# Kernel tuning notes

Hardware: AMD Instinct MI355X
Metric: run time of the kernel (lower is better)

The kernel has to match this reference:

```python
import jax, jax.numpy as jnp
import numpy as np

# pywt db4 reconstruction low-pass (rec_lo) coefficients.
_H = np.array([
    0.23037781330885523, 0.7148465705525415, 0.6308807679295904,
    -0.02798376941698385, -0.18703481171888114, 0.030841381835986965,
    0.032883011666982945, -0.010597401784997278], dtype=np.float64)
# pywt dec_lo = _H[::-1]; conv (flipped) correlation kernel = dec_lo[::-1] = _H.
_FLO = _H
# dec_hi[k] = (-1)^(7-k) * _H[k]; correlation kernel = dec_hi[::-1] -> (-1)^k * _H[7-k].
_FHI = np.array([(-1.0) ** k * _H[7 - k] for k in range(8)])
_FILT = jnp.asarray(np.stack([_FLO, _FHI])[:, None, :], dtype=jnp.float32)  # [2,1,8]
_PAD = 7  # filter_len - 1
_LEVEL = 4


def _dwt_step(sig):
    """One pywt dwt level, mode='symmetric'. sig: [N, L] -> (cA, cD), each [N, (L+7)//2]."""
    # symmetric (half-sample) extension by filter_len-1 each side, drop first sample
    # so that stride-2 VALID correlation reproduces pywt's output phase/length.
    xp = jnp.pad(sig, ((0, 0), (_PAD, _PAD)), mode='symmetric')[:, 1:]
    out = jax.lax.conv_general_dilated(
        xp[:, None, :], _FILT, window_strides=(2,), padding='VALID',
        dimension_numbers=('NCH', 'OIH', 'NCH'))  # [N, 2, (L+7)//2]
    return out[:, 0, :], out[:, 1, :]


def setup_inputs() -> dict:
    key = jax.random.key(0)
    x = jax.random.normal(key, (64, 4096, 32), dtype=jnp.float32)  # [B, L, C]
    return {"x": x}


def reference(x):
    """Faithful batched version of pywt.wavedec(x[i,:,j], 'db4', 'symmetric', level=4).
    Returns tuple (cA4, cD4, cD3, cD2, cD1), each [B, C, scale_len]."""
    B, L, C = x.shape
    sig = jnp.transpose(x, (0, 2, 1)).reshape(B * C, L)
    details = []
    for _ in range(_LEVEL):
        sig, cd = _dwt_step(sig)
        details.append(cd)
    coeffs = [sig] + details[::-1]  # [cA_L, cD_L, ..., cD_1] like pywt.wavedec
    return tuple(c.reshape(B, C, c.shape[-1]) for c in coeffs)
```

## Files before the change

kernel.cpp:

```cpp
#include <hip/hip_runtime.h>


#define NT 256
#define NCHB 2

#define LPX 634
#define LP1 322
#define LP2 166
#define LP3 86
#define CDP1 314
#define CDP2 154
#define CDP3 82
#define CDP4 40
#define CAP4 40

#define L0C 4096
#define L1C 2051
#define L2C 1029
#define L3C 518
#define L4C 262
#define SC 2048

#define OFF_CD4 ((size_t)SC * L4C)
#define OFF_CD3 ((size_t)2 * SC * L4C)
#define OFF_CD2 (OFF_CD3 + (size_t)SC * L3C)
#define OFF_CD1 (OFF_CD2 + (size_t)SC * L2C)

__device__ __forceinline__ void filt8(
    const float w0, const float w1, const float w2, const float w3,
    const float w4, const float w5, const float w6, const float w7,
    float& a, float& d) {
    constexpr float FLO[8] = {
        0.23037781330885523f,  0.7148465705525415f,  0.6308807679295904f,
        -0.02798376941698385f, -0.18703481171888114f, 0.030841381835986965f,
        0.032883011666982945f, -0.010597401784997278f};
    constexpr float FHI[8] = {
        -0.010597401784997278f, -0.032883011666982945f, 0.030841381835986965f,
        0.18703481171888114f,  -0.02798376941698385f,  -0.6308807679295904f,
        0.7148465705525415f,   -0.23037781330885523f};
    float a0 = FLO[0] * w0;
    a0 = fmaf(FLO[1], w1, a0); a0 = fmaf(FLO[2], w2, a0); a0 = fmaf(FLO[3], w3, a0);
    float a1 = FLO[4] * w4;
    a1 = fmaf(FLO[5], w5, a1); a1 = fmaf(FLO[6], w6, a1); a1 = fmaf(FLO[7], w7, a1);
    a = a0 + a1;
    float d0 = FHI[0] * w0;
    d0 = fmaf(FHI[1], w1, d0); d0 = fmaf(FHI[2], w2, d0); d0 = fmaf(FHI[3], w3, d0);
    float d1 = FHI[4] * w4;
    d1 = fmaf(FHI[5], w5, d1); d1 = fmaf(FHI[6], w6, d1); d1 = fmaf(FHI[7], w7, d1);
    d = d0 + d1;
}

template <int R, bool LAST>
__device__ __forceinline__ void level_run(
    const float* __restrict__ src, int PS, int srclo,
    float* __restrict__ dst, int PD, int DL,
    int lo, int hi,
    float* __restrict__ cdbuf, int CDP,
    float* __restrict__ cabuf,
    int c, int slot) {
    const int span = hi - lo;
    int i0r = slot * R;
    if (i0r > span - R) i0r = span - R;
    const int i0 = lo + i0r;

    const float2* row2 = reinterpret_cast<const float2*>(src + c * PS);
    int p = i0 - (srclo >> 1);
    float2 f0 = row2[p], f1 = row2[p + 1], f2 = row2[p + 2];
    float* drow = LAST ? nullptr : dst + c * PD;
    float* cdrow = cdbuf + c * CDP - lo;
    float* carow = LAST ? cabuf + c * CAP4 - lo : nullptr;

#pragma unroll
    for (int r = 0; r < R; ++r) {
        const float2 f3 = row2[p + 3 + r];
        const int i = i0 + r;
        float a, d;
        filt8(f0.x, f0.y, f1.x, f1.y, f2.x, f2.y, f3.x, f3.y, a, d);

        if constexpr (!LAST) {
            drow[i - lo + 6] = a;
            if (lo == 0 && i < 6) drow[5 - i] = a;
            if (hi == DL && i >= DL - 7) drow[(2 * DL - 1 - i) - lo + 6] = a;
        } else {
            carow[i] = a;
        }
        cdrow[i] = d;
        f0 = f1; f1 = f2; f2 = f3;
    }
}

__device__ __forceinline__ void dump_rows(
    const float* __restrict__ buf, int pitch, int bufLo,
    float* __restrict__ gbase, int rowLen, int ownLo, int ownHi, int tid) {
    const int span = ownHi - ownLo;
#pragma unroll
    for (int c2 = 0; c2 < NCHB; ++c2) {
        float* g = gbase + (size_t)c2 * rowLen + ownLo;
        const float* s = buf + c2 * pitch + (ownLo - bufLo);
        for (int i = tid; i < span; i += NT) g[i] = s[i];
    }
}

__global__ __launch_bounds__(NT, 8) void fused_dwt_kernel(
    const float* __restrict__ x, float* __restrict__ out) {
    __shared__ __align__(16) float bx[NCHB * LPX];
    __shared__ __align__(16) float b1[NCHB * LP1];
    __shared__ __align__(16) float b2[NCHB * LP2];
    __shared__ __align__(16) float b3[NCHB * LP3];
    __shared__ __align__(16) float cd1[NCHB * CDP1];
    __shared__ __align__(16) float cd2[NCHB * CDP2];
    __shared__ __align__(16) float cd3[NCHB * CDP3];
    __shared__ __align__(16) float cd4[NCHB * CDP4];
    __shared__ __align__(16) float ca4[NCHB * CAP4];

    const int bid = blockIdx.x;
    const int work = (bid & 7) * 1024 + (bid >> 3);
    const int cg = work & 15;
    const int tile = (work >> 4) & 7;
    const int b = work >> 7;

    const int tid = threadIdx.x;
    const int c = tid & 1;
    const int slot = tid >> 1;
    const int c0 = cg * 2;
    const int sigB = b * 32 + c0;

    const int lo4 = 33 * tile, hi4 = min(L4C, lo4 + 33);
    const int lo3 = max(0, 2 * lo4 - 6), hi3 = min(L3C, 2 * hi4);
    const int lo2 = max(0, 2 * lo3 - 6), hi2 = min(L2C, 2 * hi3);
    const int lo1 = max(0, 2 * lo2 - 6), hi1 = min(L1C, 2 * hi2);
    const int lox = max(0, 2 * lo1 - 6), hix = min(L0C, 2 * hi1);

    const float* xb = x + (size_t)b * (L0C * 32) + c0;
    const int npair = (hix - lox) >> 1;
    for (int q = tid; q < npair; q += NT) {
        const int j = q << 1;
        const int t = lox + j;
        const float2 va = *reinterpret_cast<const float2*>(xb + (size_t)t * 32);
        const float2 vb = *reinterpret_cast<const float2*>(xb + (size_t)(t + 1) * 32);
        const float avv[2] = {va.x, va.y};
        const float bvv[2] = {vb.x, vb.y};
#pragma unroll
        for (int hh = 0; hh < NCHB; ++hh)
            *reinterpret_cast<float2*>(bx + hh * LPX + 6 + j) = make_float2(avv[hh], bvv[hh]);
        if (lox == 0 && t < 6) {
#pragma unroll
            for (int hh = 0; hh < NCHB; ++hh) {
                bx[hh * LPX + 5 - t] = avv[hh];
                if (t + 1 < 6) bx[hh * LPX + 4 - t] = bvv[hh];
            }
        }
        if (hix == L0C && t + 1 >= L0C - 7) {
#pragma unroll
            for (int hh = 0; hh < NCHB; ++hh) {
                if (t >= L0C - 7) bx[hh * LPX + (2 * L0C - 1 - t) - lox + 6] = avv[hh];
                bx[hh * LPX + (2 * L0C - 2 - t) - lox + 6] = bvv[hh];
            }
        }
    }
    __syncthreads();

    float* gca4 = out + (size_t)sigB * L4C;
    float* gcd4 = out + OFF_CD4 + (size_t)sigB * L4C;
    float* gcd3 = out + OFF_CD3 + (size_t)sigB * L3C;
    float* gcd2 = out + OFF_CD2 + (size_t)sigB * L2C;
    float* gcd1 = out + OFF_CD1 + (size_t)sigB * L1C;

    const int o1lo = tile ? 264 * tile - 34 : 0;
    const int o1hi = (tile == 7) ? L1C : 264 * tile + 230;
    const int o2lo = tile ? 132 * tile - 10 : 0;
    const int o2hi = (tile == 7) ? L2C : 132 * tile + 122;
    const int o3lo = tile ? 66 * tile - 2 : 0;
    const int o3hi = (tile == 7) ? L3C : 66 * tile + 64;

    level_run<3, false>(bx, LPX, lox, b1, LP1, L1C, lo1, hi1, cd1, CDP1, nullptr, c, slot);
    __syncthreads();
    level_run<2, false>(b1, LP1, lo1, b2, LP2, L2C, lo2, hi2, cd2, CDP2, nullptr, c, slot);
    __syncthreads();
    level_run<1, false>(b2, LP2, lo2, b3, LP3, L3C, lo3, hi3, cd3, CDP3, nullptr, c, slot);
    __syncthreads();
    level_run<1, true>(b3, LP3, lo3, nullptr, 0, L4C, lo4, hi4, cd4, CDP4, ca4, c, slot);
    __syncthreads();

    dump_rows(cd1, CDP1, lo1, gcd1, L1C, o1lo, o1hi, tid);
    dump_rows(cd2, CDP2, lo2, gcd2, L2C, o2lo, o2hi, tid);
    dump_rows(cd3, CDP3, lo3, gcd3, L3C, o3lo, o3hi, tid);
    dump_rows(cd4, CDP4, lo4, gcd4, L4C, lo4, hi4, tid);
    dump_rows(ca4, CAP4, lo4, gca4, L4C, lo4, hi4, tid);
}

extern "C" void kernel_launch(void* const* d_in, const int* in_sizes, int n_in,
                              void* d_out, int out_size, void* d_ws, size_t ws_size,
                              hipStream_t stream) {
    (void)in_sizes; (void)n_in; (void)d_ws; (void)ws_size; (void)out_size;
    const float* x = (const float*)d_in[0];
    float* out = (float*)d_out;
    fused_dwt_kernel<<<dim3(8192), dim3(NT), 0, stream>>>(x, out);
}
```

Baseline: 32.90 us.

## Process four channels per block with larger per-thread runs and interleaved stores

Each block now handles four channels instead of two, halving the grid and loading input as float4 rows. Per-thread run lengths grow to 6/4/2/2 outputs with paired float2 LDS writes and a tail path. Boundary mirroring is specialised to edge tiles only via a template flag. Each level's detail coefficients are written to global memory right after its barrier, so the writes overlap later levels; occupancy hint drops to 5 waves because LDS use doubles.

New measurement: 30.11 us. -8.5%, faster.

```diff
diff --git a/kernel.cpp b/kernel.cpp
--- a/kernel.cpp
+++ b/kernel.cpp
@@ -2,7 +2,7 @@
 
 
 #define NT 256
-#define NCHB 2
+#define NCHB 4
 
 #define LPX 634
 #define LP1 322
@@ -21,10 +21,10 @@
 #define L4C 262
 #define SC 2048
 
-#define OFF_CD4 ((size_t)SC * L4C)
-#define OFF_CD3 ((size_t)2 * SC * L4C)
-#define OFF_CD2 (OFF_CD3 + (size_t)SC * L3C)
-#define OFF_CD1 (OFF_CD2 + (size_t)SC * L2C)
+#define OFF_CD4 (SC * L4C)
+#define OFF_CD3 (2 * SC * L4C)
+#define OFF_CD2 (OFF_CD3 + SC * L3C)
+#define OFF_CD1 (OFF_CD2 + SC * L2C)
 
 __device__ __forceinline__ void filt8(
     const float w0, const float w1, const float w2, const float w3,
@@ -50,7 +50,7 @@
     d = d0 + d1;
 }
 
-template <int R, bool LAST>
+template <int R, bool MG, bool LAST>
 __device__ __forceinline__ void level_run(
     const float* __restrict__ src, int PS, int srclo,
     float* __restrict__ dst, int PD, int DL,
@@ -58,34 +58,67 @@
     float* __restrict__ cdbuf, int CDP,
     float* __restrict__ cabuf,
     int c, int slot) {
+    static_assert((R & 1) == 0, "R must be even");
     const int span = hi - lo;
-    int i0r = slot * R;
-    if (i0r > span - R) i0r = span - R;
-    const int i0 = lo + i0r;
-
-    const float2* row2 = reinterpret_cast<const float2*>(src + c * PS);
-    int p = i0 - (srclo >> 1);
+    const int nrun = span / R;
+    bool tail = false;
+    int i0;
+    if (slot < nrun) {
+        i0 = lo + slot * R;
+    } else if (slot == nrun && nrun * R < span) {
+        i0 = lo + ((span - R) & ~1);
+        tail = (span & 1) != 0;
+    } else {
+        return;
+    }
+
+    const float* rowb = src + c * PS;
+    const float2* row2 = reinterpret_cast<const float2*>(rowb);
+    const int p = i0 - (srclo >> 1);
     float2 f0 = row2[p], f1 = row2[p + 1], f2 = row2[p + 2];
-    float* drow = LAST ? nullptr : dst + c * PD;
-    float* cdrow = cdbuf + c * CDP - lo;
-    float* carow = LAST ? cabuf + c * CAP4 - lo : nullptr;
-
+
+    float* dbase = LAST ? nullptr : dst + c * PD;
+    float* cdbase = cdbuf + c * CDP;
+    float* cabase = LAST ? cabuf + c * CAP4 : nullptr;
+
+    float ap = 0.f, dp = 0.f;
 #pragma unroll
     for (int r = 0; r < R; ++r) {
         const float2 f3 = row2[p + 3 + r];
         const int i = i0 + r;
         float a, d;
         filt8(f0.x, f0.y, f1.x, f1.y, f2.x, f2.y, f3.x, f3.y, a, d);
-
+        if (r & 1) {
+            const int w = i - 1 - lo;
+            if constexpr (!LAST)
+                *reinterpret_cast<float2*>(dbase + w + 6) = make_float2(ap, a);
+            else
+                *reinterpret_cast<float2*>(cabase + w) = make_float2(ap, a);
+            *reinterpret_cast<float2*>(cdbase + w) = make_float2(dp, d);
+        } else {
+            ap = a; dp = d;
+        }
+        if constexpr (MG && !LAST) {
+            if (lo == 0 && i < 6) dbase[5 - i] = a;
+            if (hi == DL && i >= DL - 7) dbase[(2 * DL - 1 - i) - lo + 6] = a;
+        }
+        f0 = f1; f1 = f2; f2 = f3;
+    }
+    if (tail) {
+        const int i = hi - 1;
+        const float* s = rowb + 6 - srclo;
+        float a, d;
+        filt8(s[2*i-6], s[2*i-5], s[2*i-4], s[2*i-3],
+              s[2*i-2], s[2*i-1], s[2*i],   s[2*i+1], a, d);
         if constexpr (!LAST) {
-            drow[i - lo + 6] = a;
-            if (lo == 0 && i < 6) drow[5 - i] = a;
-            if (hi == DL && i >= DL - 7) drow[(2 * DL - 1 - i) - lo + 6] = a;
+            dbase[i - lo + 6] = a;
+            if constexpr (MG) {
+                if (hi == DL && i >= DL - 7) dbase[(2 * DL - 1 - i) - lo + 6] = a;
+            }
         } else {
-            carow[i] = a;
-        }
-        cdrow[i] = d;
-        f0 = f1; f1 = f2; f2 = f3;
+            cabase[i - lo] = a;
+        }
+        cdbase[i - lo] = d;
     }
 }
 
@@ -93,15 +126,59 @@
     const float* __restrict__ buf, int pitch, int bufLo,
     float* __restrict__ gbase, int rowLen, int ownLo, int ownHi, int tid) {
     const int span = ownHi - ownLo;
+    const int n2 = span >> 1;
+    const int off = ownLo - bufLo;
 #pragma unroll
     for (int c2 = 0; c2 < NCHB; ++c2) {
-        float* g = gbase + (size_t)c2 * rowLen + ownLo;
-        const float* s = buf + c2 * pitch + (ownLo - bufLo);
-        for (int i = tid; i < span; i += NT) g[i] = s[i];
-    }
-}
-
-__global__ __launch_bounds__(NT, 8) void fused_dwt_kernel(
+        const float2* s2 = reinterpret_cast<const float2*>(buf + c2 * pitch + off);
+        float* g = gbase + c2 * rowLen + ownLo;
+        for (int k = tid; k < n2; k += NT) {
+            const float2 v = s2[k];
+            g[2 * k] = v.x;
+            g[2 * k + 1] = v.y;
+        }
+        if ((span & 1) && tid == 0) g[span - 1] = buf[c2 * pitch + off + span - 1];
+    }
+}
+
+template <bool MG>
+__device__ __forceinline__ void cascade(
+    const float* bx, float* b1, float* b2, float* b3,
+    float* cd1, float* cd2, float* cd3, float* cd4, float* ca4,
+    float* __restrict__ out, int sigB, int tile, int c, int slot, int tid,
+    int lox, int lo1, int hi1, int lo2, int hi2, int lo3, int hi3,
+    int lo4, int hi4) {
+    const int o1lo = tile ? 264 * tile - 34 : 0;
+    const int o1hi = (tile == 7) ? L1C : 264 * tile + 230;
+    const int o2lo = tile ? 132 * tile - 10 : 0;
+    const int o2hi = (tile == 7) ? L2C : 132 * tile + 122;
+    const int o3lo = tile ? 66 * tile - 2 : 0;
+    const int o3hi = (tile == 7) ? L3C : 66 * tile + 64;
+
+    level_run<6, MG, false>(bx, LPX, lox, b1, LP1, L1C, lo1, hi1, cd1, CDP1,
+                            nullptr, c, slot);
+    __syncthreads();
+
+    dump_rows(cd1, CDP1, lo1, out + OFF_CD1 + sigB * L1C, L1C, o1lo, o1hi, tid);
+    level_run<4, MG, false>(b1, LP1, lo1, b2, LP2, L2C, lo2, hi2, cd2, CDP2,
+                            nullptr, c, slot);
+    __syncthreads();
+
+    dump_rows(cd2, CDP2, lo2, out + OFF_CD2 + sigB * L2C, L2C, o2lo, o2hi, tid);
+    level_run<2, MG, false>(b2, LP2, lo2, b3, LP3, L3C, lo3, hi3, cd3, CDP3,
+                            nullptr, c, slot);
+    __syncthreads();
+
+    dump_rows(cd3, CDP3, lo3, out + OFF_CD3 + sigB * L3C, L3C, o3lo, o3hi, tid);
+    level_run<2, MG, true>(b3, LP3, lo3, nullptr, 0, L4C, lo4, hi4, cd4, CDP4,
+                           ca4, c, slot);
+    __syncthreads();
+
+    dump_rows(cd4, CDP4, lo4, out + OFF_CD4 + sigB * L4C, L4C, lo4, hi4, tid);
+    dump_rows(ca4, CAP4, lo4, out + sigB * L4C, L4C, lo4, hi4, tid);
+}
+
+__global__ __launch_bounds__(NT, 5) void fused_dwt_kernel(
     const float* __restrict__ x, float* __restrict__ out) {
     __shared__ __align__(16) float bx[NCHB * LPX];
     __shared__ __align__(16) float b1[NCHB * LP1];
@@ -114,15 +191,15 @@
     __shared__ __align__(16) float ca4[NCHB * CAP4];
 
     const int bid = blockIdx.x;
-    const int work = (bid & 7) * 1024 + (bid >> 3);
-    const int cg = work & 15;
-    const int tile = (work >> 4) & 7;
-    const int b = work >> 7;
+    const int work = (bid & 7) * 512 + (bid >> 3);
+    const int cg = work & 7;
+    const int tile = (work >> 3) & 7;
+    const int b = work >> 6;
 
     const int tid = threadIdx.x;
-    const int c = tid & 1;
-    const int slot = tid >> 1;
-    const int c0 = cg * 2;
+    const int c = tid & 3;
+    const int slot = tid >> 2;
+    const int c0 = cg * 4;
     const int sigB = b * 32 + c0;
 
     const int lo4 = 33 * tile, hi4 = min(L4C, lo4 + 33);
@@ -131,62 +208,42 @@
     const int lo1 = max(0, 2 * lo2 - 6), hi1 = min(L1C, 2 * hi2);
     const int lox = max(0, 2 * lo1 - 6), hix = min(L0C, 2 * hi1);
 
-    const float* xb = x + (size_t)b * (L0C * 32) + c0;
+    const float* xb = x + b * (L0C * 32) + c0;
     const int npair = (hix - lox) >> 1;
     for (int q = tid; q < npair; q += NT) {
         const int j = q << 1;
         const int t = lox + j;
-        const float2 va = *reinterpret_cast<const float2*>(xb + (size_t)t * 32);
-        const float2 vb = *reinterpret_cast<const float2*>(xb + (size_t)(t + 1) * 32);
-        const float avv[2] = {va.x, va.y};
-        const float bvv[2] = {vb.x, vb.y};
+        const float4 va = *reinterpret_cast<const float4*>(xb + t * 32);
+        const float4 vb = *reinterpret_cast<const float4*>(xb + t * 32 + 32);
+        const float av[4] = {va.x, va.y, va.z, va.w};
+        const float bv[4] = {vb.x, vb.y, vb.z, vb.w};
 #pragma unroll
         for (int hh = 0; hh < NCHB; ++hh)
-            *reinterpret_cast<float2*>(bx + hh * LPX + 6 + j) = make_float2(avv[hh], bvv[hh]);
+            *reinterpret_cast<float2*>(bx + hh * LPX + 6 + j) =
+                make_float2(av[hh], bv[hh]);
         if (lox == 0 && t < 6) {
 #pragma unroll
             for (int hh = 0; hh < NCHB; ++hh) {
-                bx[hh * LPX + 5 - t] = avv[hh];
-                if (t + 1 < 6) bx[hh * LPX + 4 - t] = bvv[hh];
+                bx[hh * LPX + 5 - t] = av[hh];
+                if (t + 1 < 6) bx[hh * LPX + 4 - t] = bv[hh];
             }
         }
         if (hix == L0C && t + 1 >= L0C - 7) {
 #pragma unroll
             for (int hh = 0; hh < NCHB; ++hh) {
-                if (t >= L0C - 7) bx[hh * LPX + (2 * L0C - 1 - t) - lox + 6] = avv[hh];
-                bx[hh * LPX + (2 * L0C - 2 - t) - lox + 6] = bvv[hh];
+                if (t >= L0C - 7) bx[hh * LPX + (2 * L0C - 1 - t) - lox + 6] = av[hh];
+                bx[hh * LPX + (2 * L0C - 2 - t) - lox + 6] = bv[hh];
             }
         }
     }
     __syncthreads();
 
-    float* gca4 = out + (size_t)sigB * L4C;
-    float* gcd4 = out + OFF_CD4 + (size_t)sigB * L4C;
-    float* gcd3 = out + OFF_CD3 + (size_t)sigB * L3C;
-    float* gcd2 = out + OFF_CD2 + (size_t)sigB * L2C;
-    float* gcd1 = out + OFF_CD1 + (size_t)sigB * L1C;
-
-    const int o1lo = tile ? 264 * tile - 34 : 0;
-    const int o1hi = (tile == 7) ? L1C : 264 * tile + 230;
-    const int o2lo = tile ? 132 * tile - 10 : 0;
-    const int o2hi = (tile == 7) ? L2C : 132 * tile + 122;
-    const int o3lo = tile ? 66 * tile - 2 : 0;
-    const int o3hi = (tile == 7) ? L3C : 66 * tile + 64;
-
-    level_run<3, false>(bx, LPX, lox, b1, LP1, L1C, lo1, hi1, cd1, CDP1, nullptr, c, slot);
-    __syncthreads();
-    level_run<2, false>(b1, LP1, lo1, b2, LP2, L2C, lo2, hi2, cd2, CDP2, nullptr, c, slot);
-    __syncthreads();
-    level_run<1, false>(b2, LP2, lo2, b3, LP3, L3C, lo3, hi3, cd3, CDP3, nullptr, c, slot);
-    __syncthreads();
-    level_run<1, true>(b3, LP3, lo3, nullptr, 0, L4C, lo4, hi4, cd4, CDP4, ca4, c, slot);
-    __syncthreads();
-
-    dump_rows(cd1, CDP1, lo1, gcd1, L1C, o1lo, o1hi, tid);
-    dump_rows(cd2, CDP2, lo2, gcd2, L2C, o2lo, o2hi, tid);
-    dump_rows(cd3, CDP3, lo3, gcd3, L3C, o3lo, o3hi, tid);
-    dump_rows(cd4, CDP4, lo4, gcd4, L4C, lo4, hi4, tid);
-    dump_rows(ca4, CAP4, lo4, gca4, L4C, lo4, hi4, tid);
+    if (tile == 0 || tile == 7)
+        cascade<true>(bx, b1, b2, b3, cd1, cd2, cd3, cd4, ca4, out, sigB, tile,
+                      c, slot, tid, lox, lo1, hi1, lo2, hi2, lo3, hi3, lo4, hi4);
+    else
+        cascade<false>(bx, b1, b2, b3, cd1, cd2, cd3, cd4, ca4, out, sigB, tile,
+                       c, slot, tid, lox, lo1, hi1, lo2, hi2, lo3, hi3, lo4, hi4);
 }
 
 extern "C" void kernel_launch(void* const* d_in, const int* in_sizes, int n_in,
@@ -195,5 +252,5 @@
     (void)in_sizes; (void)n_in; (void)d_ws; (void)ws_size; (void)out_size;
     const float* x = (const float*)d_in[0];
     float* out = (float*)d_out;
-    fused_dwt_kernel<<<dim3(8192), dim3(NT), 0, stream>>>(x, out);
-}
+    fused_dwt_kernel<<<dim3(4096), dim3(NT), 0, stream>>>(x, out);
+}
```
